# Optimization experiments

Hardware: AMD Instinct MI355X
Metric: run time of the kernel (lower is better)

Reference implementation:

```python
import jax, jax.numpy as jnp
import numpy as np

N_COUNTS = 6  # pyramid levels (original + 5 sum-pools)


def _sum_pool2(x):
    # 2x2x2 sum pooling (AvgPool3d with divisor_override=1)
    B, C, D, H, W = x.shape
    return x.reshape(B, C, D // 2, 2, H // 2, 2, W // 2, 2).sum(axis=(3, 5, 7))


def _forward(image, bounds):
    n = N_COUNTS
    q = jnp.log(2.0 ** jnp.arange(n, dtype=jnp.float32))  # (S,)
    qs = q.sum()
    q2s = (q * q).sum()
    qs2 = qs * qs
    kf = bounds.astype(jnp.float32)  # (K,)
    # prefactor a: 1 for k==1 (entropy branch), else 1/(k-1); inf at k==1 masked by where
    a = jnp.where(bounds == 1, 1.0, 1.0 / jnp.where(bounds == 1, jnp.inf, kf - 1.0))

    # normalizer b = sum of nonzero entries of finest map == total sum
    b = image.sum(axis=(2, 3, 4))  # (B, C)

    maps = [image]
    for _ in range(n - 1):
        maps.append(_sum_pool2(maps[-1]))

    ps = []
    for m in maps:
        x = m.reshape(m.shape[0], m.shape[1], -1)  # (B, C, V)
        mask = x != 0
        xn = x / b[:, :, None]
        safe = jnp.where(mask, xn, 1.0)  # 1.0 placeholder at zeros, masked out below
        # generic branch (k != 1): p = log(sum over nonzero of (x/b)**k)
        pw = safe[:, :, :, None] ** kf  # (B, C, V, K)
        s = jnp.sum(jnp.where(mask[..., None], pw, 0.0), axis=2)  # (B, C, K)
        p_gen = jnp.log(s)
        # k == 1 branch: p = sum over nonzero of xn * log(xn)
        p_one = jnp.sum(jnp.where(mask, xn * jnp.log(safe), 0.0), axis=2)  # (B, C)
        ps.append(jnp.where(bounds == 1, p_one[:, :, None], p_gen))

    p_all = jnp.stack(ps, axis=-1)  # (B, C, K, S)
    # least-squares slope of p vs q; a00 = min(S, ql) = n
    num = n * jnp.einsum('bcks,s->bck', p_all, q) - p_all.sum(axis=-1) * qs
    den = n * q2s - qs2
    return a * num / den  # (B, C, K)


def setup_inputs() -> dict:
    key = jax.random.key(0)
    k1, _ = jax.random.split(key)
    image = jax.random.uniform(k1, (2, 3, 128, 128, 128), dtype=jnp.float32)
    bounds = jnp.arange(8, dtype=jnp.int32) - 2  # [-2..5]
    return {"image": image, "bounds": bounds}


def reference(image, bounds):
    return _forward(image, bounds)
```

## Files before the change

### kernel.cpp

```cpp
#include <hip/hip_runtime.h>

#define CHVOL (128*128*128)

__device__ __forceinline__ void accum9(float* a, float x) {
    bool nz = (x != 0.0f);
    float u = nz ? __builtin_amdgcn_rcpf(x) : 0.0f;
    float l = nz ? __logf(x) : 0.0f;
    float x2 = x * x;
    float x4 = x2 * x2;
    a[0] = fmaf(u, u, a[0]);
    a[1] += u;
    a[2] += nz ? 1.0f : 0.0f;
    a[3] += x;
    a[4] += x2;
    a[5] = fmaf(x2, x, a[5]);
    a[6] += x4;
    a[7] = fmaf(x4, x, a[7]);
    a[8] = fmaf(x, l, a[8]);
}

template<int NS>
__device__ __forceinline__ void block_reduce(float* acc, float* red, int t) {
    #pragma unroll
    for (int s = 0; s < NS; ++s) {
        float v = acc[s];
        v += __shfl_down(v, 32, 64);
        v += __shfl_down(v, 16, 64);
        v += __shfl_down(v, 8, 64);
        v += __shfl_down(v, 4, 64);
        v += __shfl_down(v, 2, 64);
        v += __shfl_down(v, 1, 64);
        if ((t & 63) == 0) red[(t >> 6) * NS + s] = v;
    }
    __syncthreads();
}

__global__ __launch_bounds__(256) void k_main(const float* __restrict__ img,
                                              float* __restrict__ part,
                                              float* __restrict__ l3map) {
    __shared__ float zm[256];
    __shared__ float red[36 * 4];

    const int t  = threadIdx.x;
    const int l  = t & 63, w = t >> 6;
    const int r  = blockIdx.x;
    const int ch = blockIdx.y;
    const int ry = r & 15, rz = r >> 4;
    const float* base = img + (size_t)ch * CHVOL + rz * (8 * 16384) + ry * (8 * 128);

    float acc[36];
    #pragma unroll
    for (int j = 0; j < 36; ++j) acc[j] = 0.0f;

    const int x5 = l & 31;
    const int y  = ((l >> 5) & 1) | (w << 1);
    const float* tbase = base + y * 128 + x5 * 4;

    float4 v[8];
    #pragma unroll
    for (int i = 0; i < 8; ++i) v[i] = *(const float4*)(tbase + i * 16384);

    float d0 = 0.0f, d1 = 0.0f;
    float ca = 0.0f, cb = 0.0f;
    #pragma unroll
    for (int i = 0; i < 8; ++i) {
        accum9(acc, v[i].x); accum9(acc, v[i].y); accum9(acc, v[i].z); accum9(acc, v[i].w);
        float a = v[i].x + v[i].y, b = v[i].z + v[i].w;
        a += __shfl_xor(a, 32, 64);
        b += __shfl_xor(b, 32, 64);
        if ((i & 1) == 0) { ca = a; cb = b; }
        else {
            float A = ca + a, B = cb + b;
            accum9(acc + 9, A); accum9(acc + 9, B);
            if (i < 4) d0 += A + B; else d1 += A + B;
        }
    }
    #pragma unroll
    for (int j = 9; j < 18; ++j) acc[j] *= 0.5f;

    if ((l >> 5) == 0) {
        zm[w * 64 + x5]      = d0;
        zm[w * 64 + 32 + x5] = d1;
    }
    __syncthreads();

    if (t < 128) {
        int x = t & 31, zpp = (t >> 5) & 1, ypp = t >> 6;
        float s = zm[(2 * ypp) * 64 + zpp * 32 + x] + zm[(2 * ypp + 1) * 64 + zpp * 32 + x];
        accum9(acc + 18, s);
    }
    if (t < 16) {
        float s = 0.0f;
        #pragma unroll
        for (int q = 0; q < 8; ++q)
            s += zm[q * 32 + 2 * t] + zm[q * 32 + 2 * t + 1];
        accum9(acc + 27, s);
        l3map[(size_t)ch * 4096 + rz * 256 + ry * 16 + t] = s;
    }

    block_reduce<36>(acc, red, t);
    if (t < 36)
        part[((size_t)ch * 36 + t) * 256 + r] =
            red[t] + red[36 + t] + red[72 + t] + red[108 + t];
}

__global__ __launch_bounds__(256) void k_pyr(const float* __restrict__ part,
                                             const float* __restrict__ l3map,
                                             const int* __restrict__ bounds,
                                             float* __restrict__ out) {
    __shared__ float red[36 * 4];
    __shared__ float sst[54];
    __shared__ float M4[512];

    const int t  = threadIdx.x;
    const int ch = blockIdx.x;

    float acc[36];
    #pragma unroll
    for (int j = 0; j < 36; ++j)
        acc[j] = part[((size_t)ch * 36 + j) * 256 + t];
    block_reduce<36>(acc, red, t);
    if (t < 36) sst[t] = red[t] + red[36 + t] + red[72 + t] + red[108 + t];
    __syncthreads();

    const float2* L3 = (const float2*)(l3map + (size_t)ch * 4096);
    float a9[9];
    #pragma unroll
    for (int j = 0; j < 9; ++j) a9[j] = 0.0f;
    #pragma unroll
    for (int i = 0; i < 2; ++i) {
        int c = t + i * 256;
        int x = c & 7, y = (c >> 3) & 7, z = c >> 6;
        const float2* p = L3 + z * 256 + y * 16 + x;
        float2 b0 = p[0], b1 = p[8], b2 = p[128], b3 = p[136];
        float s = (b0.x + b0.y) + (b1.x + b1.y) + (b2.x + b2.y) + (b3.x + b3.y);
        M4[c] = s;
        accum9(a9, s);
    }
    __syncthreads();
    block_reduce<9>(a9, red, t);
    if (t < 9) sst[36 + t] = red[t] + red[9 + t] + red[18 + t] + red[27 + t];
    __syncthreads();

    float c9[9];
    #pragma unroll
    for (int j = 0; j < 9; ++j) c9[j] = 0.0f;
    if (t < 64) {
        int x = t & 3, y = (t >> 2) & 3, z = t >> 4;
        const float2* p = (const float2*)M4 + z * 64 + y * 8 + x;
        float2 b0 = p[0], b1 = p[4], b2 = p[32], b3 = p[36];
        float s = (b0.x + b0.y) + (b1.x + b1.y) + (b2.x + b2.y) + (b3.x + b3.y);
        accum9(c9, s);
    }
    __syncthreads();
    block_reduce<9>(c9, red, t);
    if (t < 9) sst[45 + t] = red[t] + red[9 + t] + red[18 + t] + red[27 + t];
    __syncthreads();

    if (t < 8) {
        int k = bounds[t];
        const double LN2 = 0.6931471805599453094;
        double b  = (double)sst[3];
        double lb = log(b);
        double num = 0.0;
        #pragma unroll
        for (int s = 0; s < 6; ++s) {
            const float* st = sst + s * 9;
            double p;
            if (k == 1) p = ((double)st[8] - lb * (double)st[3]) / b;
            else        p = log((double)st[k + 2]) - (double)k * lb;
            num += (6.0 * s - 15.0) * LN2 * p;
        }
        double den = 105.0 * LN2 * LN2;
        double aa  = (k == 1) ? 1.0 : 1.0 / (double)(k - 1);
        out[ch * 8 + t] = (float)(aa * num / den);
    }
}

extern "C" void kernel_launch(void* const* d_in, const int* in_sizes, int n_in,
                              void* d_out, int out_size, void* d_ws, size_t ws_size,
                              hipStream_t stream) {
    const float* img    = (const float*)d_in[0];
    const int*   bounds = (const int*)d_in[1];
    float*       out    = (float*)d_out;
    float*       ws     = (float*)d_ws;

    float* part  = ws;
    float* l3map = ws + 55296;

    k_main<<<dim3(256, 6), 256, 0, stream>>>(img, part, l3map);
    k_pyr<<<6, 256, 0, stream>>>(part, l3map, bounds, out);
}
```

Measured before the change: 119.6 us.

## Enlarge per-block tile to 32^3 so all pyramid levels reduce in main kernel

Each block now covers a 32x32x32 cube with 512 threads holding 16 float4 loads each, so levels 0 through 5 are computed inside the main kernel. Levels 2 and 3 use wavefront shuffles, and levels 4 and 5 are finished by a single thread from shared memory. This removes the level-3 intermediate map and most of the second kernel's work, leaving only a small 64-lane reduction of partials. The cost is fewer blocks (384), higher register pressure from 16 outstanding float4s plus 36 accumulators, and a serial single-thread tail.

```diff
diff --git a/kernel.cpp b/kernel.cpp
--- a/kernel.cpp
+++ b/kernel.cpp
@@ -19,7 +19,7 @@
     a[8] = fmaf(x, l, a[8]);
 }
 
-template<int NS>
+template<int NS, int NW>
 __device__ __forceinline__ void block_reduce(float* acc, float* red, int t) {
     #pragma unroll
     for (int s = 0; s < NS; ++s) {
@@ -35,126 +35,128 @@
     __syncthreads();
 }
 
-__global__ __launch_bounds__(256) void k_main(const float* __restrict__ img,
-                                              float* __restrict__ part,
-                                              float* __restrict__ l3map) {
-    __shared__ float zm[256];
-    __shared__ float red[36 * 4];
+__global__ __launch_bounds__(512, 4) void k_main(const float* __restrict__ img,
+                                                 float* __restrict__ part) {
+    __shared__ float m3[64];
+    __shared__ float red[36 * 8];
 
     const int t  = threadIdx.x;
-    const int l  = t & 63, w = t >> 6;
-    const int r  = blockIdx.x;
-    const int ch = blockIdx.y;
-    const int ry = r & 15, rz = r >> 4;
-    const float* base = img + (size_t)ch * CHVOL + rz * (8 * 16384) + ry * (8 * 128);
+    const int l  = t & 63, wv = t >> 6;
+    const int xq = t & 7;
+    const int yl = (t >> 3) & 7;
+    const int y  = yl + 8 * (wv & 3);
+    const int zb = wv >> 2;
+    const int blk = blockIdx.x;
+    const int ch  = blockIdx.y;
+    const int bx = blk & 3, by = (blk >> 2) & 3, bz = blk >> 4;
+
+    const float* tb = img + (size_t)ch * CHVOL
+                    + (size_t)(bz * 32 + zb * 16) * 16384
+                    + (by * 32 + y) * 128 + bx * 32 + xq * 4;
 
     float acc[36];
     #pragma unroll
     for (int j = 0; j < 36; ++j) acc[j] = 0.0f;
 
-    const int x5 = l & 31;
-    const int y  = ((l >> 5) & 1) | (w << 1);
-    const float* tbase = base + y * 128 + x5 * 4;
+    float4 v[16];
+    #pragma unroll
+    for (int i = 0; i < 16; ++i) v[i] = *(const float4*)(tb + i * 16384);
 
-    float4 v[8];
+    float oct0, oct1;
     #pragma unroll
-    for (int i = 0; i < 8; ++i) v[i] = *(const float4*)(tbase + i * 16384);
-
-    float d0 = 0.0f, d1 = 0.0f;
-    float ca = 0.0f, cb = 0.0f;
-    #pragma unroll
-    for (int i = 0; i < 8; ++i) {
-        accum9(acc, v[i].x); accum9(acc, v[i].y); accum9(acc, v[i].z); accum9(acc, v[i].w);
-        float a = v[i].x + v[i].y, b = v[i].z + v[i].w;
-        a += __shfl_xor(a, 32, 64);
-        b += __shfl_xor(b, 32, 64);
-        if ((i & 1) == 0) { ca = a; cb = b; }
-        else {
-            float A = ca + a, B = cb + b;
-            accum9(acc + 9, A); accum9(acc + 9, B);
-            if (i < 4) d0 += A + B; else d1 += A + B;
+    for (int h = 0; h < 2; ++h) {
+        float q0 = 0.0f, q1 = 0.0f;
+        float ca = 0.0f, cb = 0.0f;
+        #pragma unroll
+        for (int i = 0; i < 8; ++i) {
+            float4 u = v[h * 8 + i];
+            accum9(acc, u.x); accum9(acc, u.y); accum9(acc, u.z); accum9(acc, u.w);
+            float a = u.x + u.y, b = u.z + u.w;
+            a += __shfl_xor(a, 8, 64);
+            b += __shfl_xor(b, 8, 64);
+            if ((i & 1) == 0) { ca = a; cb = b; }
+            else {
+                float A = ca + a, B = cb + b;
+                accum9(acc + 9, A); accum9(acc + 9, B);
+                float s = A + B;
+                if (i < 4) q0 += s; else q1 += s;
+            }
         }
+        q0 += __shfl_xor(q0, 16, 64);
+        q1 += __shfl_xor(q1, 16, 64);
+        accum9(acc + 18, q0); accum9(acc + 18, q1);
+        float o = q0 + q1;
+        o += __shfl_xor(o, 1, 64);
+        o += __shfl_xor(o, 32, 64);
+        accum9(acc + 27, o);
+        if (h == 0) oct0 = o; else oct1 = o;
     }
     #pragma unroll
-    for (int j = 9; j < 18; ++j) acc[j] *= 0.5f;
+    for (int j = 9;  j < 18; ++j) acc[j] *= 0.5f;
+    #pragma unroll
+    for (int j = 18; j < 27; ++j) acc[j] *= 0.25f;
+    #pragma unroll
+    for (int j = 27; j < 36; ++j) acc[j] *= 0.0625f;
 
-    if ((l >> 5) == 0) {
-        zm[w * 64 + x5]      = d0;
-        zm[w * 64 + 32 + x5] = d1;
+    if ((l & 57) == 0) {
+        int x3 = (l >> 1) & 3, y3 = wv & 3;
+        m3[(zb * 2 + 0) * 16 + y3 * 4 + x3] = oct0;
+        m3[(zb * 2 + 1) * 16 + y3 * 4 + x3] = oct1;
     }
     __syncthreads();
 
-    if (t < 128) {
-        int x = t & 31, zpp = (t >> 5) & 1, ypp = t >> 6;
-        float s = zm[(2 * ypp) * 64 + zpp * 32 + x] + zm[(2 * ypp + 1) * 64 + zpp * 32 + x];
-        accum9(acc + 18, s);
+    if (t == 0) {
+        float a45[18];
+        #pragma unroll
+        for (int q = 0; q < 18; ++q) a45[q] = 0.0f;
+        float s5 = 0.0f;
+        #pragma unroll
+        for (int c = 0; c < 8; ++c) {
+            int x4 = c & 1, y4 = (c >> 1) & 1, z4 = c >> 2;
+            float s = 0.0f;
+            #pragma unroll
+            for (int dz = 0; dz < 2; ++dz)
+                #pragma unroll
+                for (int dy = 0; dy < 2; ++dy)
+                    #pragma unroll
+                    for (int dx = 0; dx < 2; ++dx)
+                        s += m3[(2 * z4 + dz) * 16 + (2 * y4 + dy) * 4 + (2 * x4 + dx)];
+            accum9(a45, s);
+            s5 += s;
+        }
+        accum9(a45 + 9, s5);
+        #pragma unroll
+        for (int q = 0; q < 18; ++q)
+            part[((size_t)ch * 54 + 36 + q) * 64 + blk] = a45[q];
     }
-    if (t < 16) {
+
+    block_reduce<36, 8>(acc, red, t);
+    if (t < 36) {
         float s = 0.0f;
         #pragma unroll
-        for (int q = 0; q < 8; ++q)
-            s += zm[q * 32 + 2 * t] + zm[q * 32 + 2 * t + 1];
-        accum9(acc + 27, s);
-        l3map[(size_t)ch * 4096 + rz * 256 + ry * 16 + t] = s;
+        for (int w2 = 0; w2 < 8; ++w2) s += red[w2 * 36 + t];
+        part[((size_t)ch * 54 + t) * 64 + blk] = s;
     }
-
-    block_reduce<36>(acc, red, t);
-    if (t < 36)
-        part[((size_t)ch * 36 + t) * 256 + r] =
-            red[t] + red[36 + t] + red[72 + t] + red[108 + t];
 }
 
-__global__ __launch_bounds__(256) void k_pyr(const float* __restrict__ part,
-                                             const float* __restrict__ l3map,
-                                             const int* __restrict__ bounds,
-                                             float* __restrict__ out) {
-    __shared__ float red[36 * 4];
+__global__ __launch_bounds__(64) void k_fin(const float* __restrict__ part,
+                                            const int* __restrict__ bounds,
+                                            float* __restrict__ out) {
     __shared__ float sst[54];
-    __shared__ float M4[512];
-
     const int t  = threadIdx.x;
     const int ch = blockIdx.x;
 
-    float acc[36];
     #pragma unroll
-    for (int j = 0; j < 36; ++j)
-        acc[j] = part[((size_t)ch * 36 + j) * 256 + t];
-    block_reduce<36>(acc, red, t);
-    if (t < 36) sst[t] = red[t] + red[36 + t] + red[72 + t] + red[108 + t];
-    __syncthreads();
-
-    const float2* L3 = (const float2*)(l3map + (size_t)ch * 4096);
-    float a9[9];
-    #pragma unroll
-    for (int j = 0; j < 9; ++j) a9[j] = 0.0f;
-    #pragma unroll
-    for (int i = 0; i < 2; ++i) {
-        int c = t + i * 256;
-        int x = c & 7, y = (c >> 3) & 7, z = c >> 6;
-        const float2* p = L3 + z * 256 + y * 16 + x;
-        float2 b0 = p[0], b1 = p[8], b2 = p[128], b3 = p[136];
-        float s = (b0.x + b0.y) + (b1.x + b1.y) + (b2.x + b2.y) + (b3.x + b3.y);
-        M4[c] = s;
-        accum9(a9, s);
+    for (int j = 0; j < 54; ++j) {
+        float v = part[((size_t)ch * 54 + j) * 64 + t];
+        v += __shfl_down(v, 32, 64);
+        v += __shfl_down(v, 16, 64);
+        v += __shfl_down(v, 8, 64);
+        v += __shfl_down(v, 4, 64);
+        v += __shfl_down(v, 2, 64);
+        v += __shfl_down(v, 1, 64);
+        if (t == 0) sst[j] = v;
     }
-    __syncthreads();
-    block_reduce<9>(a9, red, t);
-    if (t < 9) sst[36 + t] = red[t] + red[9 + t] + red[18 + t] + red[27 + t];
-    __syncthreads();
-
-    float c9[9];
-    #pragma unroll
-    for (int j = 0; j < 9; ++j) c9[j] = 0.0f;
-    if (t < 64) {
-        int x = t & 3, y = (t >> 2) & 3, z = t >> 4;
-        const float2* p = (const float2*)M4 + z * 64 + y * 8 + x;
-        float2 b0 = p[0], b1 = p[4], b2 = p[32], b3 = p[36];
-        float s = (b0.x + b0.y) + (b1.x + b1.y) + (b2.x + b2.y) + (b3.x + b3.y);
-        accum9(c9, s);
-    }
-    __syncthreads();
-    block_reduce<9>(c9, red, t);
-    if (t < 9) sst[45 + t] = red[t] + red[9 + t] + red[18 + t] + red[27 + t];
     __syncthreads();
 
     if (t < 8) {
@@ -185,9 +187,8 @@
     float*       out    = (float*)d_out;
     float*       ws     = (float*)d_ws;
 
-    float* part  = ws;
-    float* l3map = ws + 55296;
+    float* part = ws;
 
-    k_main<<<dim3(256, 6), 256, 0, stream>>>(img, part, l3map);
-    k_pyr<<<6, 256, 0, stream>>>(part, l3map, bounds, out);
+    k_main<<<dim3(64, 6), 512, 0, stream>>>(img, part);
+    k_fin<<<6, 64, 0, stream>>>(part, bounds, out);
 }
```

Result: slower. 182.6 us (+52.7%).
